# Kernel optimization log

Measured on AMD Instinct MI355X. Metric: run time of the kernel, lower is better.

The kernel has to match this reference:

```python
import jax, jax.numpy as jnp
import numpy as np

DIAGNUM, MEDNUM, PRONUM, FEATDIM = 50000, 20000, 40000, 128
N1 = DIAGNUM + MEDNUM  # 70000
N2 = PRONUM + MEDNUM   # 60000
NNZ1, NNZ2 = 1_120_000, 960_000


def setup_inputs() -> dict:
    key = jax.random.key(0)
    ks = jax.random.split(key, 10)
    return {
        "adj1_rows": jax.random.randint(ks[0], (2, NNZ1), 0, N1, dtype=jnp.int32),
        "adj1_cols": jax.random.randint(ks[1], (2, NNZ1), 0, N1, dtype=jnp.int32),
        "adj1_vals": jax.random.uniform(ks[2], (2, NNZ1), dtype=jnp.float32),
        "adj2_rows": jax.random.randint(ks[3], (2, NNZ2), 0, N2, dtype=jnp.int32),
        "adj2_cols": jax.random.randint(ks[4], (2, NNZ2), 0, N2, dtype=jnp.int32),
        "adj2_vals": jax.random.uniform(ks[5], (2, NNZ2), dtype=jnp.float32),
        "dEmbed": jax.random.normal(ks[6], (DIAGNUM, FEATDIM), dtype=jnp.float32),
        "mEmbed": jax.random.normal(ks[7], (MEDNUM, FEATDIM), dtype=jnp.float32),
        "pEmbed": jax.random.normal(ks[8], (PRONUM, FEATDIM), dtype=jnp.float32),
        "inter": jax.random.uniform(ks[9], (1,), dtype=jnp.float32),
    }


def _spmm(rows, cols, vals, x, n):
    # sparse COO matmul: out[r] += vals * x[cols]
    msgs = vals[:, None] * x[cols]  # [nnz, d]
    return jax.ops.segment_sum(msgs, rows, num_segments=n)


def _gcn_layer(rows, cols, vals, x, n):
    h = _spmm(rows, cols, vals, x, n)
    h = jnp.where(h >= 0, h, 0.5 * h)  # LeakyReLU(0.5)
    return jax.nn.relu(h)              # extra F.relu in the loop


def reference(adj1_rows, adj1_cols, adj1_vals,
              adj2_rows, adj2_cols, adj2_vals,
              dEmbed, mEmbed, pEmbed, inter):
    diagnum, pronum = dEmbed.shape[0], pEmbed.shape[0]
    e1 = jnp.concatenate([dEmbed, mEmbed], axis=0)  # [N1, d]
    e2 = jnp.concatenate([pEmbed, mEmbed], axis=0)  # [N2, d]
    n1, n2 = e1.shape[0], e2.shape[0]
    # Original loops never extend lats1/lats2, so every iteration uses the
    # initial embeddings; each adj[i] contribution appears twice (j=0,1).
    g1 = jnp.zeros_like(e1)
    g2 = jnp.zeros_like(e2)
    for _j in range(2):
        for i in range(2):
            g1 = g1 + _gcn_layer(adj1_rows[i], adj1_cols[i], adj1_vals[i], e1, n1)
            g2 = g2 + _gcn_layer(adj2_rows[i], adj2_cols[i], adj2_vals[i], e2, n2)
    mEmbed_gcn_1 = g1[diagnum:]
    dEmbed_gcn = g1[:diagnum]
    mEmbed_gcn_2 = g2[pronum:]
    pEmbed_gcn = g2[:pronum]
    mEmbed_out = inter * mEmbed_gcn_1 + (1.0 - inter) * mEmbed_gcn_2
    return (mEmbed_out, dEmbed_gcn, pEmbed_gcn)
```

## Files before the change

kernel.cpp:

```cpp
#include <hip/hip_runtime.h>

#define DIAGNUM 50000
#define MEDNUM  20000
#define PRONUM  40000
#define FEATDIM 128
#define N1 (DIAGNUM + MEDNUM)
#define N2 (PRONUM + MEDNUM)
#define NNZ1 1120000
#define NNZ2 960000
#define NTOT (2 * N1 + 2 * N2)
#define NNZTOT (2 * NNZ1 + 2 * NNZ2)
#define NBUCK ((NTOT + 255) >> 8)
#define L1_THREADS 512
#define L1_CHUNK 8192
#define L1_BLOCKS ((NNZTOT + L1_CHUNK - 1) / L1_CHUNK)

typedef unsigned short ushort_t;

__device__ __forceinline__ unsigned f2bf(float f) {
    unsigned u = __float_as_uint(f);
    return (u + 0x7FFFu + ((u >> 16) & 1u)) >> 16;
}

__device__ __forceinline__ int edge_idx(int i, const int* __restrict__ a1r,
                                        const int* __restrict__ a2r) {
    if (i < 2 * NNZ1) {
        return ((i < NNZ1) ? 0 : N1) + a1r[i];
    } else {
        int j = i - 2 * NNZ1;
        return 2 * N1 + ((j < NNZ2) ? 0 : N2) + a2r[j];
    }
}

__global__ __launch_bounds__(256) void count_buckets_kernel(
        const int* __restrict__ a1r, const int* __restrict__ a2r,
        int* __restrict__ bucketCnt) {
    __shared__ int lh[NBUCK];
    for (int b = threadIdx.x; b < NBUCK; b += 256) lh[b] = 0;
    __syncthreads();
    int stride = gridDim.x * 256;
    for (int i = blockIdx.x * 256 + threadIdx.x; i < NNZTOT; i += stride)
        atomicAdd(&lh[edge_idx(i, a1r, a2r) >> 8], 1);
    __syncthreads();
    for (int b = threadIdx.x; b < NBUCK; b += 256) {
        int h = lh[b];
        if (h) atomicAdd(&bucketCnt[b], h);
    }
}

__global__ __launch_bounds__(256) void scan_buckets_kernel(
        const int* __restrict__ bucketCnt, int* __restrict__ bucketOff,
        int* __restrict__ cursor) {
    __shared__ int s[256];
    int t = threadIdx.x;
    int vals[4];
    int sum = 0;
#pragma unroll
    for (int k = 0; k < 4; k++) {
        int b = t * 4 + k;
        vals[k] = (b < NBUCK) ? bucketCnt[b] : 0;
        sum += vals[k];
    }
    s[t] = sum;
    __syncthreads();
    for (int off = 1; off < 256; off <<= 1) {
        int y = (t >= off) ? s[t - off] : 0;
        __syncthreads();
        s[t] += y;
        __syncthreads();
    }
    int run = s[t] - sum;
#pragma unroll
    for (int k = 0; k < 4; k++) {
        int b = t * 4 + k;
        if (b < NBUCK) {
            bucketOff[b] = run;
            cursor[b] = run;
            run += vals[k];
        }
    }
    if (t == 255) bucketOff[NBUCK] = run;
}

__global__ __launch_bounds__(L1_THREADS) void lvl1_scatter_kernel(
        const int* __restrict__ a1r, const int* __restrict__ a1c,
        const float* __restrict__ a1v,
        const int* __restrict__ a2r, const int* __restrict__ a2c,
        const float* __restrict__ a2v,
        int* __restrict__ cursor, int2* __restrict__ lvl1) {
    __shared__ int lh[NBUCK];
    for (int b = threadIdx.x; b < NBUCK; b += L1_THREADS) lh[b] = 0;
    __syncthreads();
    int base = blockIdx.x * L1_CHUNK;
    int end  = min(base + L1_CHUNK, NNZTOT);
    for (int i = base + threadIdx.x; i < end; i += L1_THREADS)
        atomicAdd(&lh[edge_idx(i, a1r, a2r) >> 8], 1);
    __syncthreads();
    for (int b = threadIdx.x; b < NBUCK; b += L1_THREADS) {
        int h = lh[b];
        lh[b] = h ? atomicAdd(&cursor[b], h) : 0;
    }
    __syncthreads();
    for (int i = base + threadIdx.x; i < end; i += L1_THREADS) {
        int idx, col;
        float val;
        if (i < 2 * NNZ1) {
            idx = ((i < NNZ1) ? 0 : N1) + a1r[i];
            col = a1c[i];
            val = a1v[i];
        } else {
            int j = i - 2 * NNZ1;
            idx = 2 * N1 + ((j < NNZ2) ? 0 : N2) + a2r[j];
            col = a2c[j];
            val = a2v[j];
        }
        int pos = atomicAdd(&lh[idx >> 8], 1);
        lvl1[pos] = make_int2(((idx & 255) << 17) | col, __float_as_int(val));
    }
}

__global__ __launch_bounds__(256) void lvl2_sort_kernel(
        const int2* __restrict__ lvl1, const int* __restrict__ bucketOff,
        int* __restrict__ binned, int* __restrict__ rpe) {
    __shared__ int cnt[256];
    __shared__ int sc[256];
    int b = blockIdx.x;
    int t = threadIdx.x;
    int s0 = bucketOff[b];
    int e0 = bucketOff[b + 1];
    cnt[t] = 0;
    __syncthreads();
    for (int k = s0 + t; k < e0; k += 256)
        atomicAdd(&cnt[lvl1[k].x >> 17], 1);
    __syncthreads();
    int v = cnt[t];
    sc[t] = v;
    __syncthreads();
    for (int off = 1; off < 256; off <<= 1) {
        int y = (t >= off) ? sc[t - off] : 0;
        __syncthreads();
        sc[t] += y;
        __syncthreads();
    }
    int incl = sc[t];
    int excl = incl - v;
    int idx = (b << 8) + t;
    if (idx < NTOT) rpe[idx + 1] = s0 + incl;
    cnt[t] = excl;
    __syncthreads();
    for (int k = s0 + t; k < e0; k += 256) {
        int2 rec = lvl1[k];
        int rl  = rec.x >> 17;
        int col = rec.x & 0x1FFFF;
        unsigned bf15 = f2bf(__int_as_float(rec.y)) & 0x7FFFu;
        int pos = atomicAdd(&cnt[rl], 1);
        binned[s0 + pos] = (int)((bf15 << 17) | (unsigned)col);
    }
}

#define TOT8 ((DIAGNUM + MEDNUM + PRONUM) * (FEATDIM / 8))

__global__ __launch_bounds__(256) void convert_emb_kernel(
        const float* __restrict__ dE, const float* __restrict__ mE,
        const float* __restrict__ pE,
        ushort_t* __restrict__ embd, ushort_t* __restrict__ embm,
        ushort_t* __restrict__ embp) {
    int t8 = blockIdx.x * 256 + threadIdx.x;
    if (t8 >= TOT8) return;
    long flat = (long)t8 * 8;
    const float* src;
    ushort_t* dst;
    if (flat < (long)DIAGNUM * FEATDIM) {
        src = dE + flat;                          dst = embd + flat;
    } else if (flat < (long)(DIAGNUM + MEDNUM) * FEATDIM) {
        long o = flat - (long)DIAGNUM * FEATDIM;  src = mE + o; dst = embm + o;
    } else {
        long o = flat - (long)(DIAGNUM + MEDNUM) * FEATDIM;
        src = pE + o;                             dst = embp + o;
    }
    float4 a = *reinterpret_cast<const float4*>(src);
    float4 b = *reinterpret_cast<const float4*>(src + 4);
    int4 w;
    w.x = (int)(f2bf(a.x) | (f2bf(a.y) << 16));
    w.y = (int)(f2bf(a.z) | (f2bf(a.w) << 16));
    w.z = (int)(f2bf(b.x) | (f2bf(b.y) << 16));
    w.w = (int)(f2bf(b.z) | (f2bf(b.w) << 16));
    *reinterpret_cast<int4*>(dst) = w;
}


__device__ __forceinline__ void fma8(float acc[8], float v, int4 h) {
    acc[0] = fmaf(v, __uint_as_float((unsigned)h.x << 16), acc[0]);
    acc[1] = fmaf(v, __uint_as_float((unsigned)h.x & 0xFFFF0000u), acc[1]);
    acc[2] = fmaf(v, __uint_as_float((unsigned)h.y << 16), acc[2]);
    acc[3] = fmaf(v, __uint_as_float((unsigned)h.y & 0xFFFF0000u), acc[3]);
    acc[4] = fmaf(v, __uint_as_float((unsigned)h.z << 16), acc[4]);
    acc[5] = fmaf(v, __uint_as_float((unsigned)h.z & 0xFFFF0000u), acc[5]);
    acc[6] = fmaf(v, __uint_as_float((unsigned)h.w << 16), acc[6]);
    acc[7] = fmaf(v, __uint_as_float((unsigned)h.w & 0xFFFF0000u), acc[7]);
}

__device__ __forceinline__ const ushort_t* rec_base(unsigned rec, int nlo,
                                                    const ushort_t* __restrict__ xlo,
                                                    const ushort_t* __restrict__ xhi) {
    int col = (int)(rec & 0x1FFFFu);
    return (col < nlo) ? xlo + (size_t)col * FEATDIM
                       : xhi + (size_t)(col - nlo) * FEATDIM;
}

__device__ __forceinline__ void gather8(int s, int e,
                                        const int* __restrict__ binned,
                                        int q, int sub16,
                                        const ushort_t* __restrict__ xlo,
                                        const ushort_t* __restrict__ xhi,
                                        int nlo, float acc[8]) {
    int k = s + q;
    for (; k + 4 < e; k += 8) {
        unsigned r0 = (unsigned)binned[k];
        unsigned r1 = (unsigned)binned[k + 4];
        const ushort_t* b0 = rec_base(r0, nlo, xlo, xhi);
        const ushort_t* b1 = rec_base(r1, nlo, xlo, xhi);
        int4 h0 = reinterpret_cast<const int4*>(b0)[sub16];
        int4 h1 = reinterpret_cast<const int4*>(b1)[sub16];
        fma8(acc, __uint_as_float((r0 >> 17) << 16), h0);
        fma8(acc, __uint_as_float((r1 >> 17) << 16), h1);
    }
    for (; k < e; k += 4) {
        unsigned r0 = (unsigned)binned[k];
        const ushort_t* b0 = rec_base(r0, nlo, xlo, xhi);
        int4 h0 = reinterpret_cast<const int4*>(b0)[sub16];
        fma8(acc, __uint_as_float((r0 >> 17) << 16), h0);
    }
}

__global__ __launch_bounds__(256) void fused_gcn_kernel(
        const int* __restrict__ rpe,
        const int* __restrict__ binned,
        const ushort_t* __restrict__ embd, const ushort_t* __restrict__ embm,
        const ushort_t* __restrict__ embp,
        const float* __restrict__ inter,
        float* __restrict__ out_d, float* __restrict__ out_p,
        float* __restrict__ out_m, int graph) {
    int gtid = blockIdx.x * blockDim.x + threadIdx.x;
    int w     = gtid >> 6;
    int lane  = gtid & 63;
    int q     = lane >> 4;
    int sub16 = lane & 15;

    const ushort_t *xlo, *xhi = embm;
    const int *rpA, *rpB;
    int nlo, nrows;
    if (graph) { xlo = embd; nlo = DIAGNUM; nrows = N1;
                 rpA = rpe + w; rpB = rpe + N1 + w; }
    else       { xlo = embp; nlo = PRONUM;  nrows = N2;
                 rpA = rpe + 2 * N1 + w; rpB = rpe + 2 * N1 + N2 + w; }
    if (w >= nrows) return;

    float aA[8] = {0, 0, 0, 0, 0, 0, 0, 0};
    float aB[8] = {0, 0, 0, 0, 0, 0, 0, 0};
    gather8(rpA[0], rpA[1], binned, q, sub16, xlo, xhi, nlo, aA);
    gather8(rpB[0], rpB[1], binned, q, sub16, xlo, xhi, nlo, aB);

#pragma unroll
    for (int j = 0; j < 8; j++) {
        aA[j] += __shfl_xor(aA[j], 16);
        aA[j] += __shfl_xor(aA[j], 32);
        aB[j] += __shfl_xor(aB[j], 16);
        aB[j] += __shfl_xor(aB[j], 32);
    }

    if (lane >= 16) return;

    float r[8];
#pragma unroll
    for (int j = 0; j < 8; j++)
        r[j] = 2.f * (fmaxf(aA[j], 0.f) + fmaxf(aB[j], 0.f));

    float4 lo = make_float4(r[0], r[1], r[2], r[3]);
    float4 hi = make_float4(r[4], r[5], r[6], r[7]);

    if (graph) {
        if (w < DIAGNUM) {
            float4* dst = reinterpret_cast<float4*>(out_d + (size_t)w * FEATDIM);
            dst[sub16 * 2]     = lo;
            dst[sub16 * 2 + 1] = hi;
        } else {
            float t = *inter;
            float4* dst = reinterpret_cast<float4*>(
                out_m + (size_t)(w - DIAGNUM) * FEATDIM);
            float4 o0 = dst[sub16 * 2];
            float4 o1 = dst[sub16 * 2 + 1];
            o0.x = fmaf(t, lo.x, o0.x); o0.y = fmaf(t, lo.y, o0.y);
            o0.z = fmaf(t, lo.z, o0.z); o0.w = fmaf(t, lo.w, o0.w);
            o1.x = fmaf(t, hi.x, o1.x); o1.y = fmaf(t, hi.y, o1.y);
            o1.z = fmaf(t, hi.z, o1.z); o1.w = fmaf(t, hi.w, o1.w);
            dst[sub16 * 2]     = o0;
            dst[sub16 * 2 + 1] = o1;
        }
    } else {
        if (w < PRONUM) {
            float4* dst = reinterpret_cast<float4*>(out_p + (size_t)w * FEATDIM);
            dst[sub16 * 2]     = lo;
            dst[sub16 * 2 + 1] = hi;
        } else {
            float sc = 1.0f - *inter;
            lo.x *= sc; lo.y *= sc; lo.z *= sc; lo.w *= sc;
            hi.x *= sc; hi.y *= sc; hi.z *= sc; hi.w *= sc;
            float4* dst = reinterpret_cast<float4*>(
                out_m + (size_t)(w - PRONUM) * FEATDIM);
            dst[sub16 * 2]     = lo;
            dst[sub16 * 2 + 1] = hi;
        }
    }
}


extern "C" void kernel_launch(void* const* d_in, const int* in_sizes, int n_in,
                              void* d_out, int out_size, void* d_ws, size_t ws_size,
                              hipStream_t stream) {
    const int*   a1r = (const int*)d_in[0];
    const int*   a1c = (const int*)d_in[1];
    const float* a1v = (const float*)d_in[2];
    const int*   a2r = (const int*)d_in[3];
    const int*   a2c = (const int*)d_in[4];
    const float* a2v = (const float*)d_in[5];
    const float* dE  = (const float*)d_in[6];
    const float* mE  = (const float*)d_in[7];
    const float* pE  = (const float*)d_in[8];
    const float* inter = (const float*)d_in[9];

    float* out   = (float*)d_out;
    float* out_m = out;
    float* out_d = out + (size_t)MEDNUM * FEATDIM;
    float* out_p = out_d + (size_t)DIAGNUM * FEATDIM;

    char* ws = (char*)d_ws;
    int* binned = (int*)ws;          ws += (size_t)NNZTOT * 4;
    char* regionB = ws;              ws += (size_t)NNZTOT * 8;
    int2*     lvl1 = (int2*)regionB;
    ushort_t* embd = (ushort_t*)regionB;
    ushort_t* embm = embd + (size_t)DIAGNUM * FEATDIM;
    ushort_t* embp = embm + (size_t)MEDNUM * FEATDIM;
    int* rpe       = (int*)ws;       ws += (((size_t)(NTOT + 1) * 4 + 15) & ~15ull);
    int* bucketCnt = (int*)ws;       ws += (size_t)NBUCK * 4;
    int* bucketOff = (int*)ws;       ws += (size_t)(NBUCK + 1) * 4;
    int* cursor    = (int*)ws;       ws += (size_t)NBUCK * 4;

    const int BLK = 256;

    hipMemsetAsync(bucketCnt, 0, (size_t)NBUCK * sizeof(int), stream);
    hipMemsetAsync(rpe, 0, sizeof(int), stream);

    count_buckets_kernel<<<512, BLK, 0, stream>>>(a1r, a2r, bucketCnt);
    scan_buckets_kernel<<<1, BLK, 0, stream>>>(bucketCnt, bucketOff, cursor);
    lvl1_scatter_kernel<<<L1_BLOCKS, L1_THREADS, 0, stream>>>(
        a1r, a1c, a1v, a2r, a2c, a2v, cursor, lvl1);
    lvl2_sort_kernel<<<NBUCK, BLK, 0, stream>>>(lvl1, bucketOff, binned, rpe);

    convert_emb_kernel<<<(TOT8 + BLK - 1) / BLK, BLK, 0, stream>>>(
        dE, mE, pE, embd, embm, embp);

    fused_gcn_kernel<<<(N2 + 3) / 4, BLK, 0, stream>>>(
        rpe, binned, embd, embm, embp, inter, out_d, out_p, out_m, 0);
    fused_gcn_kernel<<<(N1 + 3) / 4, BLK, 0, stream>>>(
        rpe, binned, embd, embm, embp, inter, out_d, out_p, out_m, 1);
}
```

Measured before the change: 257.1 us.

## Switch gathered embeddings and edge weights to fp16, concatenate tables, cache row indices

Edge weights and embeddings are now stored as fp16 instead of bf16. Each graph gets its own contiguous concatenated embedding table, with the med rows written twice, so the gather drops the lo/hi branch per edge. The level-1 scatter now keeps computed row indices in registers between passes instead of reloading the row arrays. Fp16 gives more mantissa but less range, the edge weight loses its sign bit (15 bits kept), and the embedding buffer grows by one med copy.

```diff
diff --git a/kernel.cpp b/kernel.cpp
--- a/kernel.cpp
+++ b/kernel.cpp
@@ -1,4 +1,5 @@
 #include <hip/hip_runtime.h>
+#include <hip/hip_fp16.h>
 
 #define DIAGNUM 50000
 #define MEDNUM  20000
@@ -13,14 +14,10 @@
 #define NBUCK ((NTOT + 255) >> 8)
 #define L1_THREADS 512
 #define L1_CHUNK 8192
+#define L1_ITERS (L1_CHUNK / L1_THREADS)
 #define L1_BLOCKS ((NNZTOT + L1_CHUNK - 1) / L1_CHUNK)
 
 typedef unsigned short ushort_t;
-
-__device__ __forceinline__ unsigned f2bf(float f) {
-    unsigned u = __float_as_uint(f);
-    return (u + 0x7FFFu + ((u >> 16) & 1u)) >> 16;
-}
 
 __device__ __forceinline__ int edge_idx(int i, const int* __restrict__ a1r,
                                         const int* __restrict__ a2r) {
@@ -93,29 +90,38 @@
     __syncthreads();
     int base = blockIdx.x * L1_CHUNK;
     int end  = min(base + L1_CHUNK, NNZTOT);
-    for (int i = base + threadIdx.x; i < end; i += L1_THREADS)
-        atomicAdd(&lh[edge_idx(i, a1r, a2r) >> 8], 1);
+    int idxv[L1_ITERS];
+    {
+        int it = 0;
+        for (int i = base + threadIdx.x; i < end; i += L1_THREADS, it++) {
+            int idx = edge_idx(i, a1r, a2r);
+            idxv[it] = idx;
+            atomicAdd(&lh[idx >> 8], 1);
+        }
+    }
     __syncthreads();
     for (int b = threadIdx.x; b < NBUCK; b += L1_THREADS) {
         int h = lh[b];
         lh[b] = h ? atomicAdd(&cursor[b], h) : 0;
     }
     __syncthreads();
-    for (int i = base + threadIdx.x; i < end; i += L1_THREADS) {
-        int idx, col;
-        float val;
-        if (i < 2 * NNZ1) {
-            idx = ((i < NNZ1) ? 0 : N1) + a1r[i];
-            col = a1c[i];
-            val = a1v[i];
-        } else {
-            int j = i - 2 * NNZ1;
-            idx = 2 * N1 + ((j < NNZ2) ? 0 : N2) + a2r[j];
-            col = a2c[j];
-            val = a2v[j];
-        }
-        int pos = atomicAdd(&lh[idx >> 8], 1);
-        lvl1[pos] = make_int2(((idx & 255) << 17) | col, __float_as_int(val));
+    {
+        int it = 0;
+        for (int i = base + threadIdx.x; i < end; i += L1_THREADS, it++) {
+            int col;
+            float val;
+            if (i < 2 * NNZ1) {
+                col = a1c[i];
+                val = a1v[i];
+            } else {
+                int j = i - 2 * NNZ1;
+                col = a2c[j];
+                val = a2v[j];
+            }
+            int idx = idxv[it];
+            int pos = atomicAdd(&lh[idx >> 8], 1);
+            lvl1[pos] = make_int2(((idx & 255) << 17) | col, __float_as_int(val));
+        }
     }
 }
 
@@ -152,92 +158,96 @@
         int2 rec = lvl1[k];
         int rl  = rec.x >> 17;
         int col = rec.x & 0x1FFFF;
-        unsigned bf15 = f2bf(__int_as_float(rec.y)) & 0x7FFFu;
+        unsigned hv = __half_as_ushort(__float2half(__int_as_float(rec.y)));
         int pos = atomicAdd(&cnt[rl], 1);
-        binned[s0 + pos] = (int)((bf15 << 17) | (unsigned)col);
+        binned[s0 + pos] = (int)((hv << 17) | (unsigned)col);
     }
 }
 
 #define TOT8 ((DIAGNUM + MEDNUM + PRONUM) * (FEATDIM / 8))
+
+__device__ __forceinline__ ushort_t f2h(float x) {
+    return __half_as_ushort(__float2half(x));
+}
 
 __global__ __launch_bounds__(256) void convert_emb_kernel(
         const float* __restrict__ dE, const float* __restrict__ mE,
         const float* __restrict__ pE,
-        ushort_t* __restrict__ embd, ushort_t* __restrict__ embm,
-        ushort_t* __restrict__ embp) {
+        ushort_t* __restrict__ emb1, ushort_t* __restrict__ emb2) {
     int t8 = blockIdx.x * 256 + threadIdx.x;
     if (t8 >= TOT8) return;
     long flat = (long)t8 * 8;
     const float* src;
     ushort_t* dst;
+    ushort_t* dst2 = nullptr;
     if (flat < (long)DIAGNUM * FEATDIM) {
-        src = dE + flat;                          dst = embd + flat;
+        src = dE + flat;
+        dst = emb1 + flat;
     } else if (flat < (long)(DIAGNUM + MEDNUM) * FEATDIM) {
-        long o = flat - (long)DIAGNUM * FEATDIM;  src = mE + o; dst = embm + o;
+        long o = flat - (long)DIAGNUM * FEATDIM;
+        src = mE + o;
+        dst  = emb1 + (long)DIAGNUM * FEATDIM + o;
+        dst2 = emb2 + (long)PRONUM * FEATDIM + o;
     } else {
         long o = flat - (long)(DIAGNUM + MEDNUM) * FEATDIM;
-        src = pE + o;                             dst = embp + o;
+        src = pE + o;
+        dst = emb2 + o;
     }
     float4 a = *reinterpret_cast<const float4*>(src);
     float4 b = *reinterpret_cast<const float4*>(src + 4);
     int4 w;
-    w.x = (int)(f2bf(a.x) | (f2bf(a.y) << 16));
-    w.y = (int)(f2bf(a.z) | (f2bf(a.w) << 16));
-    w.z = (int)(f2bf(b.x) | (f2bf(b.y) << 16));
-    w.w = (int)(f2bf(b.z) | (f2bf(b.w) << 16));
+    w.x = (int)((unsigned)f2h(a.x) | ((unsigned)f2h(a.y) << 16));
+    w.y = (int)((unsigned)f2h(a.z) | ((unsigned)f2h(a.w) << 16));
+    w.z = (int)((unsigned)f2h(b.x) | ((unsigned)f2h(b.y) << 16));
+    w.w = (int)((unsigned)f2h(b.z) | ((unsigned)f2h(b.w) << 16));
     *reinterpret_cast<int4*>(dst) = w;
+    if (dst2) *reinterpret_cast<int4*>(dst2) = w;
 }
 
 
 __device__ __forceinline__ void fma8(float acc[8], float v, int4 h) {
-    acc[0] = fmaf(v, __uint_as_float((unsigned)h.x << 16), acc[0]);
-    acc[1] = fmaf(v, __uint_as_float((unsigned)h.x & 0xFFFF0000u), acc[1]);
-    acc[2] = fmaf(v, __uint_as_float((unsigned)h.y << 16), acc[2]);
-    acc[3] = fmaf(v, __uint_as_float((unsigned)h.y & 0xFFFF0000u), acc[3]);
-    acc[4] = fmaf(v, __uint_as_float((unsigned)h.z << 16), acc[4]);
-    acc[5] = fmaf(v, __uint_as_float((unsigned)h.z & 0xFFFF0000u), acc[5]);
-    acc[6] = fmaf(v, __uint_as_float((unsigned)h.w << 16), acc[6]);
-    acc[7] = fmaf(v, __uint_as_float((unsigned)h.w & 0xFFFF0000u), acc[7]);
-}
-
-__device__ __forceinline__ const ushort_t* rec_base(unsigned rec, int nlo,
-                                                    const ushort_t* __restrict__ xlo,
-                                                    const ushort_t* __restrict__ xhi) {
-    int col = (int)(rec & 0x1FFFFu);
-    return (col < nlo) ? xlo + (size_t)col * FEATDIM
-                       : xhi + (size_t)(col - nlo) * FEATDIM;
+    union U { int4 i; __half2 h2[4]; } u;
+    u.i = h;
+#pragma unroll
+    for (int j = 0; j < 4; j++) {
+        float2 f = __half22float2(u.h2[j]);
+        acc[2 * j]     = fmaf(v, f.x, acc[2 * j]);
+        acc[2 * j + 1] = fmaf(v, f.y, acc[2 * j + 1]);
+    }
+}
+
+__device__ __forceinline__ float rec_val(unsigned rec) {
+    return __half2float(__ushort_as_half((unsigned short)(rec >> 17)));
 }
 
 __device__ __forceinline__ void gather8(int s, int e,
                                         const int* __restrict__ binned,
                                         int q, int sub16,
-                                        const ushort_t* __restrict__ xlo,
-                                        const ushort_t* __restrict__ xhi,
-                                        int nlo, float acc[8]) {
+                                        const ushort_t* __restrict__ emb,
+                                        float acc[8]) {
     int k = s + q;
     for (; k + 4 < e; k += 8) {
         unsigned r0 = (unsigned)binned[k];
         unsigned r1 = (unsigned)binned[k + 4];
-        const ushort_t* b0 = rec_base(r0, nlo, xlo, xhi);
-        const ushort_t* b1 = rec_base(r1, nlo, xlo, xhi);
-        int4 h0 = reinterpret_cast<const int4*>(b0)[sub16];
-        int4 h1 = reinterpret_cast<const int4*>(b1)[sub16];
-        fma8(acc, __uint_as_float((r0 >> 17) << 16), h0);
-        fma8(acc, __uint_as_float((r1 >> 17) << 16), h1);
+        const int4* b0 = reinterpret_cast<const int4*>(emb + ((size_t)(r0 & 0x1FFFFu) << 7));
+        const int4* b1 = reinterpret_cast<const int4*>(emb + ((size_t)(r1 & 0x1FFFFu) << 7));
+        int4 h0 = b0[sub16];
+        int4 h1 = b1[sub16];
+        fma8(acc, rec_val(r0), h0);
+        fma8(acc, rec_val(r1), h1);
     }
     for (; k < e; k += 4) {
         unsigned r0 = (unsigned)binned[k];
-        const ushort_t* b0 = rec_base(r0, nlo, xlo, xhi);
-        int4 h0 = reinterpret_cast<const int4*>(b0)[sub16];
-        fma8(acc, __uint_as_float((r0 >> 17) << 16), h0);
+        const int4* b0 = reinterpret_cast<const int4*>(emb + ((size_t)(r0 & 0x1FFFFu) << 7));
+        int4 h0 = b0[sub16];
+        fma8(acc, rec_val(r0), h0);
     }
 }
 
 __global__ __launch_bounds__(256) void fused_gcn_kernel(
         const int* __restrict__ rpe,
         const int* __restrict__ binned,
-        const ushort_t* __restrict__ embd, const ushort_t* __restrict__ embm,
-        const ushort_t* __restrict__ embp,
+        const ushort_t* __restrict__ emb,
         const float* __restrict__ inter,
         float* __restrict__ out_d, float* __restrict__ out_p,
         float* __restrict__ out_m, int graph) {
@@ -247,19 +257,16 @@
     int q     = lane >> 4;
     int sub16 = lane & 15;
 
-    const ushort_t *xlo, *xhi = embm;
     const int *rpA, *rpB;
-    int nlo, nrows;
-    if (graph) { xlo = embd; nlo = DIAGNUM; nrows = N1;
-                 rpA = rpe + w; rpB = rpe + N1 + w; }
-    else       { xlo = embp; nlo = PRONUM;  nrows = N2;
-                 rpA = rpe + 2 * N1 + w; rpB = rpe + 2 * N1 + N2 + w; }
+    int nrows;
+    if (graph) { nrows = N1; rpA = rpe + w; rpB = rpe + N1 + w; }
+    else       { nrows = N2; rpA = rpe + 2 * N1 + w; rpB = rpe + 2 * N1 + N2 + w; }
     if (w >= nrows) return;
 
     float aA[8] = {0, 0, 0, 0, 0, 0, 0, 0};
     float aB[8] = {0, 0, 0, 0, 0, 0, 0, 0};
-    gather8(rpA[0], rpA[1], binned, q, sub16, xlo, xhi, nlo, aA);
-    gather8(rpB[0], rpB[1], binned, q, sub16, xlo, xhi, nlo, aB);
+    gather8(rpA[0], rpA[1], binned, q, sub16, emb, aA);
+    gather8(rpB[0], rpB[1], binned, q, sub16, emb, aB);
 
 #pragma unroll
     for (int j = 0; j < 8; j++) {
@@ -338,9 +345,8 @@
     int* binned = (int*)ws;          ws += (size_t)NNZTOT * 4;
     char* regionB = ws;              ws += (size_t)NNZTOT * 8;
     int2*     lvl1 = (int2*)regionB;
-    ushort_t* embd = (ushort_t*)regionB;
-    ushort_t* embm = embd + (size_t)DIAGNUM * FEATDIM;
-    ushort_t* embp = embm + (size_t)MEDNUM * FEATDIM;
+    ushort_t* emb1 = (ushort_t*)regionB;
+    ushort_t* emb2 = emb1 + (size_t)N1 * FEATDIM;
     int* rpe       = (int*)ws;       ws += (((size_t)(NTOT + 1) * 4 + 15) & ~15ull);
     int* bucketCnt = (int*)ws;       ws += (size_t)NBUCK * 4;
     int* bucketOff = (int*)ws;       ws += (size_t)(NBUCK + 1) * 4;
@@ -358,10 +364,10 @@
     lvl2_sort_kernel<<<NBUCK, BLK, 0, stream>>>(lvl1, bucketOff, binned, rpe);
 
     convert_emb_kernel<<<(TOT8 + BLK - 1) / BLK, BLK, 0, stream>>>(
-        dE, mE, pE, embd, embm, embp);
+        dE, mE, pE, emb1, emb2);
 
     fused_gcn_kernel<<<(N2 + 3) / 4, BLK, 0, stream>>>(
-        rpe, binned, embd, embm, embp, inter, out_d, out_p, out_m, 0);
+        rpe, binned, emb2, inter, out_d, out_p, out_m, 0);
     fused_gcn_kernel<<<(N1 + 3) / 4, BLK, 0, stream>>>(
-        rpe, binned, embd, embm, embp, inter, out_d, out_p, out_m, 1);
-}
+        rpe, binned, emb1, inter, out_d, out_p, out_m, 1);
+}
```

New measurement: 255.0 us. About the same (-0.8%).
